# Performance work log

Measured on AMD Instinct MI355X. Metric: run time of the kernel, lower is better.

The kernel has to match this reference:

```python
import jax, jax.numpy as jnp
import numpy as np
from math import sqrt

B, T, C = 4, 2048, 2048
H = 16
D = C // H  # head_dim = 128


def setup_inputs() -> dict:
    key = jax.random.key(0)
    ks = jax.random.split(key, 7)
    s = 1.0 / sqrt(C)
    return {
        "querys": jax.random.normal(ks[0], (B, T, C), dtype=jnp.float32),
        "keys": jax.random.normal(ks[1], (B, T, C), dtype=jnp.float32),
        "values": jax.random.normal(ks[2], (B, T, C), dtype=jnp.float32),
        "Wq": jax.random.normal(ks[3], (C, C), dtype=jnp.float32) * s,
        "bq": jnp.zeros((C,), dtype=jnp.float32),
        "Wk": jax.random.normal(ks[4], (C, C), dtype=jnp.float32) * s,
        "bk": jnp.zeros((C,), dtype=jnp.float32),
        "Wv": jax.random.normal(ks[5], (C, C), dtype=jnp.float32) * s,
        "bv": jnp.zeros((C,), dtype=jnp.float32),
        "Wo": jax.random.normal(ks[6], (C, C), dtype=jnp.float32) * s,
        "bo": jnp.zeros((C,), dtype=jnp.float32),
        "is_causal": 1,
    }


def reference(querys, keys, values, Wq, bq, Wk, bk, Wv, bv, Wo, bo, is_causal):
    # Linear projections: x @ W^T + b (torch nn.Linear convention), here W stored as [C_in, C_out]
    q = (querys @ Wq + bq).reshape(B, T, H, D)
    k = (keys @ Wk + bk).reshape(B, T, H, D)
    v = (values @ Wv + bv).reshape(B, T, H, D)
    # scores: [B, H, T, T]
    scores = jnp.einsum("bqhd,bkhd->bhqk", q, k) / sqrt(D)
    if is_causal:
        mask = jnp.tril(jnp.ones((T, T), dtype=bool))  # allowed positions
        scores = jnp.where(mask, scores, -jnp.inf)
    weights = jax.nn.softmax(scores, axis=-1)
    attn = jnp.einsum("bhqk,bkhd->bqhd", weights, v).reshape(B, T, C)
    return attn @ Wo + bo
```

## Files before the change

### kernel.cpp

```cpp
#include <hip/hip_runtime.h>
#include <hip/hip_bf16.h>
#include <stdint.h>

#define BB 4
#define TT 2048
#define CC 2048
#define HH 16
#define DD 128
#define MM (BB*TT)

typedef __attribute__((ext_vector_type(8))) short bh8;
typedef __attribute__((ext_vector_type(4))) float fx4;

__device__ inline ushort f2bf(float x) {
    union { float f; uint32_t u; } c; c.f = x;
    uint32_t lsb = (c.u >> 16) & 1u;
    return (ushort)((c.u + 0x7fffu + lsb) >> 16);
}

__device__ inline void async16(const void* g, void* l) {
    __builtin_amdgcn_global_load_lds(
        (const __attribute__((address_space(1))) uint32_t*)g,
        (__attribute__((address_space(3))) uint32_t*)l, 16, 0, 0);
}

__global__ __launch_bounds__(256) void convert3_k(
    const float* __restrict__ i0, const float* __restrict__ i1,
    const float* __restrict__ i2,
    ushort* __restrict__ o0, ushort* __restrict__ o1, ushort* __restrict__ o2,
    int n)
{
    const float* in; ushort* out;
    switch (blockIdx.y) {
        case 0:  in = i0; out = o0; break;
        case 1:  in = i1; out = o1; break;
        default: in = i2; out = o2; break;
    }
    int i = (int)(blockIdx.x * 256 + threadIdx.x) * 4;
    if (i + 3 < n) {
        float4 v = *(const float4*)&in[i];
        ushort4 o;
        o.x = f2bf(v.x); o.y = f2bf(v.y); o.z = f2bf(v.z); o.w = f2bf(v.w);
        *(ushort4*)&out[i] = o;
    }
}

__global__ __launch_bounds__(256) void transpose4_w_k(
    const float* __restrict__ w0, const float* __restrict__ w1,
    const float* __restrict__ w2, const float* __restrict__ w3,
    ushort* __restrict__ t0, ushort* __restrict__ t1,
    ushort* __restrict__ t2, ushort* __restrict__ t3)
{
    const float* W; ushort* Wt;
    switch (blockIdx.z) {
        case 0:  W = w0; Wt = t0; break;
        case 1:  W = w1; Wt = t1; break;
        case 2:  W = w2; Wt = t2; break;
        default: W = w3; Wt = t3; break;
    }
    __shared__ __align__(16) ushort tile[32][33];
    const int n0 = blockIdx.x * 32, k0 = blockIdx.y * 32;
    const int tx = threadIdx.x, ty = threadIdx.y;
#pragma unroll
    for (int r = 0; r < 32; r += 8)
        tile[ty + r][tx] = f2bf(W[(size_t)(k0 + ty + r) * CC + n0 + tx]);
    __syncthreads();
    const int tid = ty * 32 + tx;
    const int p = tid & 15;
    const int row = tid >> 4;
#pragma unroll
    for (int rr = 0; rr < 2; ++rr) {
        const int n_row = row + rr * 16;
        ushort2 w2;
        w2.x = tile[2 * p][n_row];
        w2.y = tile[2 * p + 1][n_row];
        *(ushort2*)&Wt[(size_t)(n0 + n_row) * CC + k0 + 2 * p] = w2;
    }
}

template<int OUTF>
__device__ __forceinline__ void gemm_body(
    char (*Gsm)[65536],
    const ushort* A, const ushort* Bt, const float* bias, void* Cv, float osc)
{
    const int tid = (int)threadIdx.x;
    const int lane = tid & 63, wave = tid >> 6;
    const int fr = lane & 15, fg = lane >> 4;
    const int wm = wave >> 2, wn = wave & 3;

    const int bid = (int)blockIdx.x;
    const int xcd = bid & 7, local = bid >> 3;
    const int m_tile = xcd * 4 + (local >> 3);
    const int n_tile = local & 7;
    const int m0 = m_tile * 256, n0 = n_tile * 256;

    const ushort* Ag = A  + (size_t)m0 * CC;
    const ushort* Bg = Bt + (size_t)n0 * CC;
    const int nt = CC / 64;

    auto STAGE_G = [&](int t, int g) {
        if (t >= nt) return;
        const int khalf = g >> 1, isB = g & 1;
        char* base = Gsm[t & 1] + isB * 32768 + khalf * 16384;
        const ushort* src = isB ? Bg : Ag;
        const int kbase = t * 64 + khalf * 32;
#pragma unroll
        for (int l = 0; l < 2; ++l) {
            const int u = l * 512 + tid;
            const int j = u >> 3, s = u & 7;
            const int ek = s ^ (j & 7);
            const int e = (ek >> 2) & 1, ks = ek & 3;
            async16(src + (size_t)(2 * j + e) * CC + kbase + ks * 8,
                    base + u * 16);
        }
    };

    const int slot = ((((fr & 1) << 2) | fg) ^ ((fr >> 1) & 7));
    const int offA = (wm * 64 + (fr >> 1)) * 128 + slot * 16;
    const int offB = 32768 + (wn * 32 + (fr >> 1)) * 128 + slot * 16;

    fx4 acc[8][4];
#pragma unroll
    for (int i = 0; i < 8; ++i)
#pragma unroll
        for (int j = 0; j < 4; ++j)
            acc[i][j] = (fx4){0.f, 0.f, 0.f, 0.f};

#pragma unroll
    for (int g = 0; g < 4; ++g) STAGE_G(0, g);
    STAGE_G(1, 0);

#pragma unroll 1
    for (int t = 0; t < nt; ++t) {
        const char* kb = Gsm[t & 1];
#pragma unroll
        for (int kk = 0; kk < 2; ++kk) {
            if (kk == 0) {
                if (t == nt - 1) {
                    asm volatile("s_waitcnt vmcnt(0)" ::: "memory");
                } else {
                    asm volatile("s_waitcnt vmcnt(2)" ::: "memory");
                }
                __builtin_amdgcn_sched_barrier(0);
                __builtin_amdgcn_s_barrier();
                __builtin_amdgcn_sched_barrier(0);
            }

            const char* ka = kb + kk * 16384;
            const char* kbB = kb + kk * 16384;
            bh8 afr[4], bfr[4];

#pragma unroll
            for (int nf = 0; nf < 4; ++nf)
                bfr[nf] = *(const bh8*)(kbB + offB + nf * 1024);
#pragma unroll
            for (int i = 0; i < 4; ++i)
                afr[i] = *(const bh8*)(ka + offA + i * 1024);
            STAGE_G(t + 1, kk ? 3 : 1);

            __builtin_amdgcn_sched_barrier(0);
            __builtin_amdgcn_s_barrier();
            __builtin_amdgcn_sched_barrier(0);

            __builtin_amdgcn_s_setprio(1);
#pragma unroll
            for (int i = 0; i < 4; ++i)
#pragma unroll
                for (int nf = 0; nf < 4; ++nf)
                    acc[i][nf] = __builtin_amdgcn_mfma_f32_16x16x32_bf16(
                        afr[i], bfr[nf], acc[i][nf], 0, 0, 0);
            __builtin_amdgcn_s_setprio(0);

#pragma unroll
            for (int i = 0; i < 4; ++i)
                afr[i] = *(const bh8*)(ka + offA + (4 + i) * 1024);
            if (kk) STAGE_G(t + 2, 0);
            else    STAGE_G(t + 1, 2);

            __builtin_amdgcn_sched_barrier(0);
            __builtin_amdgcn_s_barrier();
            __builtin_amdgcn_sched_barrier(0);

            __builtin_amdgcn_s_setprio(1);
#pragma unroll
            for (int i = 0; i < 4; ++i)
#pragma unroll
                for (int nf = 0; nf < 4; ++nf)
                    acc[4 + i][nf] = __builtin_amdgcn_mfma_f32_16x16x32_bf16(
                        afr[i], bfr[nf], acc[4 + i][nf], 0, 0, 0);
            __builtin_amdgcn_s_setprio(0);
        }
    }

    if (OUTF == 2) {
        ushort* Vt = (ushort*)Cv;
#pragma unroll
        for (int nf = 0; nf < 4; ++nf) {
            const int col = n0 + wn * 64 + nf * 16 + fr;
            const int h = col >> 7, d = col & 127;
            const float bv = bias[col];
#pragma unroll
            for (int mfp = 0; mfp < 4; ++mfp) {
                const int rowb = m0 + wm * 128 + mfp * 32;
                const int b = rowb >> 11;
                const int tloc = (rowb & (TT - 1)) + fg * 8;
                union { ushort u[8]; uint4 v; } pk;
#pragma unroll
                for (int r = 0; r < 4; ++r) {
                    pk.u[r]     = f2bf(acc[2 * mfp][nf][r] + bv);
                    pk.u[4 + r] = f2bf(acc[2 * mfp + 1][nf][r] + bv);
                }
                *(uint4*)&Vt[((size_t)((b * HH + h) * DD + d)) * TT + tloc] = pk.v;
            }
        }
        return;
    }

#pragma unroll
    for (int nf = 0; nf < 4; ++nf) {
        const int col = n0 + wn * 64 + nf * 16 + fr;
        const float bv = bias[col];
#pragma unroll
        for (int mf = 0; mf < 8; ++mf) {
            const int row = m0 + wm * 128 + mf * 16 + fg * 4;
#pragma unroll
            for (int r = 0; r < 4; ++r) {
                float v = (acc[mf][nf][r] + bv) * osc;
                if (OUTF)
                    ((float*)Cv)[(size_t)(row + r) * CC + col] = v;
                else
                    ((ushort*)Cv)[(size_t)(row + r) * CC + col] = f2bf(v);
            }
        }
    }
}

__global__ __launch_bounds__(512, 2) void gemm_qkv_k(
    const ushort* __restrict__ Xq, const ushort* __restrict__ Xk,
    const ushort* __restrict__ Xv,
    const ushort* __restrict__ WqT, const ushort* __restrict__ WkT,
    const ushort* __restrict__ WvT,
    const float* __restrict__ bq, const float* __restrict__ bk,
    const float* __restrict__ bv,
    ushort* __restrict__ Qb, ushort* __restrict__ Kb, ushort* __restrict__ Vt)
{
    __shared__ __align__(16) char Gsm[2][65536];
    if (blockIdx.y == 0) {
        gemm_body<0>(Gsm, Xq, WqT, bq, Qb, 0.12751789836306614f);
    } else if (blockIdx.y == 1) {
        gemm_body<0>(Gsm, Xk, WkT, bk, Kb, 1.0f);
    } else {
        gemm_body<2>(Gsm, Xv, WvT, bv, Vt, 1.0f);
    }
}

__global__ __launch_bounds__(512, 2) void gemm_o_k(
    const ushort* __restrict__ A, const ushort* __restrict__ Bt,
    const float* __restrict__ bias, float* __restrict__ Cv)
{
    __shared__ __align__(16) char Gsm[2][65536];
    gemm_body<1>(Gsm, A, Bt, bias, Cv, 1.0f);
}

__global__ __launch_bounds__(512, 4) void flash_attn_k(
    const ushort* __restrict__ Qm, const ushort* __restrict__ Km,
    const ushort* __restrict__ Vt, ushort* __restrict__ Om,
    const int* __restrict__ causal_p)
{
    __shared__ __align__(16) char Ksm[2][16384];
    __shared__ __align__(16) char Vsm[2][16384];

    const int tid = (int)threadIdx.x;
    const int lane = tid & 63, wave = tid >> 6;
    const int fr = lane & 15, fg = lane >> 4;
    const int causal = causal_p[0];

    const int d_raw = (int)blockIdx.x + 8 * ((int)blockIdx.y + 16 * (int)blockIdx.z);
    const int xcd = d_raw & 7, jj = d_raw >> 3;
    const int head_lin = xcd * 8 + (jj & 7);
    const int pi = jj >> 3;
    const int h = head_lin & 15, b = head_lin >> 4;

    const ushort* Qp = Qm + (size_t)b * TT * CC + h * DD;
    const ushort* Kp = Km + (size_t)b * TT * CC + h * DD;
    const ushort* Vp = Vt + (size_t)(b * HH + h) * DD * TT;
    ushort* Op = Om + (size_t)b * TT * CC + h * DD;

    const bh8 onesf = {0x3F80, 0x3F80, 0x3F80, 0x3F80,
                       0x3F80, 0x3F80, 0x3F80, 0x3F80};

    auto STAGE = [&](int ti, int buf) {
        const int kv0 = ti * 64;
        {
            const int r0 = tid >> 4, s0 = tid & 15;
            async16(Kp + (size_t)(kv0 + r0) * CC + (s0 ^ (r0 & 15)) * 8,
                    Ksm[buf] + tid * 16);
            async16(Kp + (size_t)(kv0 + 32 + r0) * CC + (s0 ^ (r0 & 15)) * 8,
                    Ksm[buf] + 8192 + tid * 16);
        }
        {
            const int d0 = tid >> 3, s0 = tid & 7;
            async16(Vp + (size_t)d0 * TT + kv0 + (s0 ^ (d0 & 7)) * 8,
                    Vsm[buf] + tid * 16);
            async16(Vp + (size_t)(64 + d0) * TT + kv0 + (s0 ^ (d0 & 7)) * 8,
                    Vsm[buf] + 8192 + tid * 16);
        }
    };

#pragma unroll 1
    for (int pp = 0; pp < 2; ++pp) {
        const int tile = pp ? (15 - pi) : pi;
        const int q0 = tile * 128;
        const int qbase = q0 + wave * 16;
        const int q_idx = qbase + fr;

        bh8 qf[4];
#pragma unroll
        for (int s = 0; s < 4; ++s)
            qf[s] = *(const bh8*)&Qp[(size_t)(qbase + fr) * CC + s * 32 + fg * 8];

        fx4 o[8];
#pragma unroll
        for (int jn = 0; jn < 8; ++jn) o[jn] = (fx4){0.f, 0.f, 0.f, 0.f};
        fx4 o_l = (fx4){0.f, 0.f, 0.f, 0.f};

        const int nfull  = causal ? (q0 >> 6) : (TT / 64);
        const int ntiles = causal ? (nfull + 2) : (TT / 64);

        STAGE(0, 0);
#pragma unroll 1
        for (int t = 0; t < ntiles; ++t) {
            asm volatile("s_waitcnt vmcnt(0)" ::: "memory");
            __builtin_amdgcn_sched_barrier(0);
            __builtin_amdgcn_s_barrier();
            __builtin_amdgcn_sched_barrier(0);
            if (t + 1 < ntiles) STAGE(t + 1, (t + 1) & 1);

            const int kv0 = t * 64;
            const char* kb = Ksm[t & 1];
            const char* vb = Vsm[t & 1];
            const bool domask = causal && (t >= nfull);
            const bool active = !domask || (kv0 <= qbase + 15);

            if (active) {
                fx4 s4[4];
#pragma unroll
                for (int j = 0; j < 4; ++j) s4[j] = (fx4){0.f, 0.f, 0.f, 0.f};
                __builtin_amdgcn_s_setprio(1);
#pragma unroll
                for (int st = 0; st < 4; ++st) {
                    bh8 kf[4];
#pragma unroll
                    for (int j = 0; j < 4; ++j)
                        kf[j] = *(const bh8*)(kb + (j * 16 + fr) * 256 +
                                              ((st * 64 + fg * 16) ^ (fr << 4)));
#pragma unroll
                    for (int j = 0; j < 4; ++j)
                        s4[j] = __builtin_amdgcn_mfma_f32_16x16x32_bf16(
                            kf[j], qf[st], s4[j], 0, 0, 0);
                }
                __builtin_amdgcn_s_setprio(0);

#pragma unroll
                for (int g = 0; g < 2; ++g) {
                    float pg[2][4];
#pragma unroll
                    for (int j2 = 0; j2 < 2; ++j2) {
                        const int jb = g * 2 + j2;
#pragma unroll
                        for (int r = 0; r < 4; ++r) {
                            float v = s4[jb][r];
                            if (domask && (kv0 + jb * 16 + fg * 4 + r > q_idx))
                                v = -1e30f;
                            pg[j2][r] = exp2f(v);
                        }
                    }
                    union { uint u[4]; bh8 h; } pk;
                    asm("v_cvt_pk_bf16_f32 %0, %1, %2"
                        : "=v"(pk.u[0]) : "v"(pg[0][0]), "v"(pg[0][1]));
                    asm("v_cvt_pk_bf16_f32 %0, %1, %2"
                        : "=v"(pk.u[1]) : "v"(pg[0][2]), "v"(pg[0][3]));
                    asm("v_cvt_pk_bf16_f32 %0, %1, %2"
                        : "=v"(pk.u[2]) : "v"(pg[1][0]), "v"(pg[1][1]));
                    asm("v_cvt_pk_bf16_f32 %0, %1, %2"
                        : "=v"(pk.u[3]) : "v"(pg[1][2]), "v"(pg[1][3]));
                    const bh8 pf = pk.h;

                    o_l = __builtin_amdgcn_mfma_f32_16x16x32_bf16(
                        pf, onesf, o_l, 0, 0, 0);

                    __builtin_amdgcn_s_setprio(1);
#pragma unroll
                    for (int jn = 0; jn < 8; ++jn) {
                        bh8 vf = *(const bh8*)(vb + (jn * 16 + fr) * 128 +
                                               ((g * 64 + fg * 16) ^ ((fr & 7) << 4)));
                        o[jn] = __builtin_amdgcn_mfma_f32_16x16x32_bf16(
                            pf, vf, o[jn], 0, 0, 0);
                    }
                    __builtin_amdgcn_s_setprio(0);
                }
            }
        }

#pragma unroll
        for (int r = 0; r < 4; ++r) {
            const float inv = 1.0f / o_l[r];
            const size_t rowoff = (size_t)(qbase + fg * 4 + r) * CC;
#pragma unroll
            for (int jn = 0; jn < 8; ++jn)
                Op[rowoff + jn * 16 + fr] = f2bf(o[jn][r] * inv);
        }
    }
}

extern "C" void kernel_launch(void* const* d_in, const int* in_sizes, int n_in,
                              void* d_out, int out_size, void* d_ws, size_t ws_size,
                              hipStream_t stream)
{
    (void)in_sizes; (void)n_in; (void)out_size;
    const float* querys = (const float*)d_in[0];
    const float* keys   = (const float*)d_in[1];
    const float* values = (const float*)d_in[2];
    const float* Wq = (const float*)d_in[3];
    const float* bq = (const float*)d_in[4];
    const float* Wk = (const float*)d_in[5];
    const float* bk = (const float*)d_in[6];
    const float* Wv = (const float*)d_in[7];
    const float* bv = (const float*)d_in[8];
    const float* Wo = (const float*)d_in[9];
    const float* bo = (const float*)d_in[10];
    const int* is_causal = (const int*)d_in[11];

    const size_t WBYTES = (size_t)CC * CC * 2;
    const size_t XBYTES = (size_t)MM * CC * 2;
    if (ws_size < 4 * WBYTES + 4 * XBYTES) return;

    uint8_t* ws = (uint8_t*)d_ws;
    ushort* WqT = (ushort*)(ws);
    ushort* WkT = (ushort*)(ws + WBYTES);
    ushort* WvT = (ushort*)(ws + 2 * WBYTES);
    ushort* WoT = (ushort*)(ws + 3 * WBYTES);
    uint8_t* act = ws + 4 * WBYTES;
    ushort* Xq = (ushort*)(act);
    ushort* Xk = (ushort*)(act + XBYTES);
    ushort* Xv = (ushort*)(act + 2 * XBYTES);
    ushort* Qb = (ushort*)(act + 3 * XBYTES);
    ushort* Kb = Xq;
    ushort* Vt = Xk;
    ushort* Ob = Xv;

    dim3 tb(32, 8);
    transpose4_w_k<<<dim3(CC / 32, CC / 32, 4), tb, 0, stream>>>(
        Wq, Wk, Wv, Wo, WqT, WkT, WvT, WoT);

    const int nX = MM * CC;
    convert3_k<<<dim3(nX / 4 / 256, 3), 256, 0, stream>>>(
        querys, keys, values, Xq, Xk, Xv, nX);

    gemm_qkv_k<<<dim3((MM / 256) * (CC / 256), 3), 512, 0, stream>>>(
        Xq, Xk, Xv, WqT, WkT, WvT, bq, bk, bv, Qb, Kb, Vt);

    dim3 ga(8, HH, BB);
    flash_attn_k<<<ga, 512, 0, stream>>>(Qb, Kb, Vt, Ob, is_causal);

    gemm_o_k<<<dim3((MM / 256) * (CC / 256)), 512, 0, stream>>>(
        Ob, WoT, bo, (float*)d_out);
}
```

Before: 425.3 us.

## Process both paired causal tiles in a single KV sweep with 32 rows per wave

Instead of looping twice over the KV sequence (once for tile pi, once for tile 15-pi), waves 0-3 handle tile pi and waves 4-7 handle tile 15-pi in one shared sweep. Each wave now owns 32 query rows, so every K and V fragment read from LDS feeds two MFMAs. This removes the second round of KV staging for the short tile and improves LDS-to-MFMA reuse. In exchange, register use doubles for the accumulators, and the waves on the short tile sit idle through the later iterations of the sweep.

```diff
diff --git a/kernel.cpp b/kernel.cpp
--- a/kernel.cpp
+++ b/kernel.cpp
@@ -307,75 +307,89 @@
         }
     };
 
+    const int tile_sel = (wave < 4) ? pi : (15 - pi);
+    const int q0 = tile_sel * 128;
+    const int qbase = q0 + (wave & 3) * 32;
+
+    bh8 qf[2][4];
+#pragma unroll
+    for (int qq = 0; qq < 2; ++qq)
+#pragma unroll
+        for (int s = 0; s < 4; ++s)
+            qf[qq][s] = *(const bh8*)&Qp[(size_t)(qbase + qq * 16 + fr) * CC +
+                                         s * 32 + fg * 8];
+
+    fx4 o[2][8];
+#pragma unroll
+    for (int qq = 0; qq < 2; ++qq)
+#pragma unroll
+        for (int jn = 0; jn < 8; ++jn) o[qq][jn] = (fx4){0.f, 0.f, 0.f, 0.f};
+    fx4 o_l[2];
+    o_l[0] = (fx4){0.f, 0.f, 0.f, 0.f};
+    o_l[1] = (fx4){0.f, 0.f, 0.f, 0.f};
+
+    const int nt_sweep = causal ? ((15 - pi) * 2 + 2) : (TT / 64);
+    const int my_nfull = causal ? (q0 >> 6) : nt_sweep;
+    const int my_nt    = causal ? (my_nfull + 2) : nt_sweep;
+
+    STAGE(0, 0);
 #pragma unroll 1
-    for (int pp = 0; pp < 2; ++pp) {
-        const int tile = pp ? (15 - pi) : pi;
-        const int q0 = tile * 128;
-        const int qbase = q0 + wave * 16;
-        const int q_idx = qbase + fr;
-
-        bh8 qf[4];
-#pragma unroll
-        for (int s = 0; s < 4; ++s)
-            qf[s] = *(const bh8*)&Qp[(size_t)(qbase + fr) * CC + s * 32 + fg * 8];
-
-        fx4 o[8];
-#pragma unroll
-        for (int jn = 0; jn < 8; ++jn) o[jn] = (fx4){0.f, 0.f, 0.f, 0.f};
-        fx4 o_l = (fx4){0.f, 0.f, 0.f, 0.f};
-
-        const int nfull  = causal ? (q0 >> 6) : (TT / 64);
-        const int ntiles = causal ? (nfull + 2) : (TT / 64);
-
-        STAGE(0, 0);
-#pragma unroll 1
-        for (int t = 0; t < ntiles; ++t) {
-            asm volatile("s_waitcnt vmcnt(0)" ::: "memory");
-            __builtin_amdgcn_sched_barrier(0);
-            __builtin_amdgcn_s_barrier();
-            __builtin_amdgcn_sched_barrier(0);
-            if (t + 1 < ntiles) STAGE(t + 1, (t + 1) & 1);
-
-            const int kv0 = t * 64;
-            const char* kb = Ksm[t & 1];
-            const char* vb = Vsm[t & 1];
-            const bool domask = causal && (t >= nfull);
-            const bool active = !domask || (kv0 <= qbase + 15);
-
-            if (active) {
-                fx4 s4[4];
-#pragma unroll
-                for (int j = 0; j < 4; ++j) s4[j] = (fx4){0.f, 0.f, 0.f, 0.f};
-                __builtin_amdgcn_s_setprio(1);
-#pragma unroll
-                for (int st = 0; st < 4; ++st) {
-                    bh8 kf[4];
-#pragma unroll
-                    for (int j = 0; j < 4; ++j)
-                        kf[j] = *(const bh8*)(kb + (j * 16 + fr) * 256 +
-                                              ((st * 64 + fg * 16) ^ (fr << 4)));
-#pragma unroll
-                    for (int j = 0; j < 4; ++j)
-                        s4[j] = __builtin_amdgcn_mfma_f32_16x16x32_bf16(
-                            kf[j], qf[st], s4[j], 0, 0, 0);
+    for (int t = 0; t < nt_sweep; ++t) {
+        asm volatile("s_waitcnt vmcnt(0)" ::: "memory");
+        __builtin_amdgcn_sched_barrier(0);
+        __builtin_amdgcn_s_barrier();
+        __builtin_amdgcn_sched_barrier(0);
+        if (t + 1 < nt_sweep) STAGE(t + 1, (t + 1) & 1);
+
+        const int kv0 = t * 64;
+        const char* kb = Ksm[t & 1];
+        const char* vb = Vsm[t & 1];
+        const bool domask = causal && (t >= my_nfull);
+        const bool active = (t < my_nt) && (!domask || (kv0 <= qbase + 31));
+
+        if (active) {
+            fx4 s4[2][4];
+#pragma unroll
+            for (int qq = 0; qq < 2; ++qq)
+#pragma unroll
+                for (int j = 0; j < 4; ++j) s4[qq][j] = (fx4){0.f, 0.f, 0.f, 0.f};
+            __builtin_amdgcn_s_setprio(1);
+#pragma unroll
+            for (int st = 0; st < 4; ++st) {
+                bh8 kf[4];
+#pragma unroll
+                for (int j = 0; j < 4; ++j)
+                    kf[j] = *(const bh8*)(kb + (j * 16 + fr) * 256 +
+                                          ((st * 64 + fg * 16) ^ (fr << 4)));
+#pragma unroll
+                for (int j = 0; j < 4; ++j) {
+                    s4[0][j] = __builtin_amdgcn_mfma_f32_16x16x32_bf16(
+                        kf[j], qf[0][st], s4[0][j], 0, 0, 0);
+                    s4[1][j] = __builtin_amdgcn_mfma_f32_16x16x32_bf16(
+                        kf[j], qf[1][st], s4[1][j], 0, 0, 0);
                 }
-                __builtin_amdgcn_s_setprio(0);
-
-#pragma unroll
-                for (int g = 0; g < 2; ++g) {
+            }
+            __builtin_amdgcn_s_setprio(0);
+
+#pragma unroll
+            for (int g = 0; g < 2; ++g) {
+                bh8 pf[2];
+#pragma unroll
+                for (int qq = 0; qq < 2; ++qq) {
+                    const int q_idx = qbase + qq * 16 + fr;
                     float pg[2][4];
 #pragma unroll
                     for (int j2 = 0; j2 < 2; ++j2) {
                         const int jb = g * 2 + j2;
 #pragma unroll
                         for (int r = 0; r < 4; ++r) {
-                            float v = s4[jb][r];
+                            float v = s4[qq][jb][r];
                             if (domask && (kv0 + jb * 16 + fg * 4 + r > q_idx))
                                 v = -1e30f;
                             pg[j2][r] = exp2f(v);
                         }
                     }
-                    union { uint u[4]; bh8 h; } pk;
+                    union { uint u[4]; bh8 hh; } pk;
                     asm("v_cvt_pk_bf16_f32 %0, %1, %2"
                         : "=v"(pk.u[0]) : "v"(pg[0][0]), "v"(pg[0][1]));
                     asm("v_cvt_pk_bf16_f32 %0, %1, %2"
@@ -384,33 +398,36 @@
                         : "=v"(pk.u[2]) : "v"(pg[1][0]), "v"(pg[1][1]));
                     asm("v_cvt_pk_bf16_f32 %0, %1, %2"
                         : "=v"(pk.u[3]) : "v"(pg[1][2]), "v"(pg[1][3]));
-                    const bh8 pf = pk.h;
-
-                    o_l = __builtin_amdgcn_mfma_f32_16x16x32_bf16(
-                        pf, onesf, o_l, 0, 0, 0);
-
-                    __builtin_amdgcn_s_setprio(1);
-#pragma unroll
-                    for (int jn = 0; jn < 8; ++jn) {
-                        bh8 vf = *(const bh8*)(vb + (jn * 16 + fr) * 128 +
-                                               ((g * 64 + fg * 16) ^ ((fr & 7) << 4)));
-                        o[jn] = __builtin_amdgcn_mfma_f32_16x16x32_bf16(
-                            pf, vf, o[jn], 0, 0, 0);
-                    }
-                    __builtin_amdgcn_s_setprio(0);
+                    pf[qq] = pk.hh;
+                    o_l[qq] = __builtin_amdgcn_mfma_f32_16x16x32_bf16(
+                        pf[qq], onesf, o_l[qq], 0, 0, 0);
                 }
+
+                __builtin_amdgcn_s_setprio(1);
+#pragma unroll
+                for (int jn = 0; jn < 8; ++jn) {
+                    bh8 vf = *(const bh8*)(vb + (jn * 16 + fr) * 128 +
+                                           ((g * 64 + fg * 16) ^ ((fr & 7) << 4)));
+                    o[0][jn] = __builtin_amdgcn_mfma_f32_16x16x32_bf16(
+                        pf[0], vf, o[0][jn], 0, 0, 0);
+                    o[1][jn] = __builtin_amdgcn_mfma_f32_16x16x32_bf16(
+                        pf[1], vf, o[1][jn], 0, 0, 0);
+                }
+                __builtin_amdgcn_s_setprio(0);
             }
         }
-
+    }
+
+#pragma unroll
+    for (int qq = 0; qq < 2; ++qq)
 #pragma unroll
         for (int r = 0; r < 4; ++r) {
-            const float inv = 1.0f / o_l[r];
-            const size_t rowoff = (size_t)(qbase + fg * 4 + r) * CC;
+            const float inv = 1.0f / o_l[qq][r];
+            const size_t rowoff = (size_t)(qbase + qq * 16 + fg * 4 + r) * CC;
 #pragma unroll
             for (int jn = 0; jn < 8; ++jn)
-                Op[rowoff + jn * 16 + fr] = f2bf(o[jn][r] * inv);
-        }
-    }
+                Op[rowoff + jn * 16 + fr] = f2bf(o[qq][jn][r] * inv);
+        }
 }
 
 extern "C" void kernel_launch(void* const* d_in, const int* in_sizes, int n_in,
```

After: 583.3 us. +37.1%, slower.

## Fuse fp32-to-bf16 activation conversion into the QKV GEMM load path

Applied to the files above, without the earlier changes.

Removes the separate conversion kernel and has the QKV GEMM read fp32 activations directly into registers, convert them with packed bf16 instructions, and write the result into LDS, with the register loads software-pipelined across k-steps. This drops a full write and re-read of three bf16 activation copies. In exchange the GEMM reads twice as many A bytes (fp32) and uses register-staged loads instead of direct global-to-LDS loads, which adds register pressure and VALU/LDS-write work inside the main loop and changes the waitcnt accounting.

```diff
diff --git a/kernel.cpp b/kernel.cpp
--- a/kernel.cpp
+++ b/kernel.cpp
@@ -24,27 +24,6 @@
         (__attribute__((address_space(3))) uint32_t*)l, 16, 0, 0);
 }
 
-__global__ __launch_bounds__(256) void convert3_k(
-    const float* __restrict__ i0, const float* __restrict__ i1,
-    const float* __restrict__ i2,
-    ushort* __restrict__ o0, ushort* __restrict__ o1, ushort* __restrict__ o2,
-    int n)
-{
-    const float* in; ushort* out;
-    switch (blockIdx.y) {
-        case 0:  in = i0; out = o0; break;
-        case 1:  in = i1; out = o1; break;
-        default: in = i2; out = o2; break;
-    }
-    int i = (int)(blockIdx.x * 256 + threadIdx.x) * 4;
-    if (i + 3 < n) {
-        float4 v = *(const float4*)&in[i];
-        ushort4 o;
-        o.x = f2bf(v.x); o.y = f2bf(v.y); o.z = f2bf(v.z); o.w = f2bf(v.w);
-        *(ushort4*)&out[i] = o;
-    }
-}
-
 __global__ __launch_bounds__(256) void transpose4_w_k(
     const float* __restrict__ w0, const float* __restrict__ w1,
     const float* __restrict__ w2, const float* __restrict__ w3,
@@ -78,10 +57,10 @@
     }
 }
 
-template<int OUTF>
+template<int OUTF, int AF32>
 __device__ __forceinline__ void gemm_body(
     char (*Gsm)[65536],
-    const ushort* A, const ushort* Bt, const float* bias, void* Cv, float osc)
+    const void* Av, const ushort* Bt, const float* bias, void* Cv, float osc)
 {
     const int tid = (int)threadIdx.x;
     const int lane = tid & 63, wave = tid >> 6;
@@ -94,7 +73,8 @@
     const int n_tile = local & 7;
     const int m0 = m_tile * 256, n0 = n_tile * 256;
 
-    const ushort* Ag = A  + (size_t)m0 * CC;
+    const ushort* Ag16 = (const ushort*)Av + (size_t)m0 * CC;
+    const float*  Ag32 = (const float*)Av  + (size_t)m0 * CC;
     const ushort* Bg = Bt + (size_t)n0 * CC;
     const int nt = CC / 64;
 
@@ -102,7 +82,7 @@
         if (t >= nt) return;
         const int khalf = g >> 1, isB = g & 1;
         char* base = Gsm[t & 1] + isB * 32768 + khalf * 16384;
-        const ushort* src = isB ? Bg : Ag;
+        const ushort* src = isB ? Bg : Ag16;
         const int kbase = t * 64 + khalf * 32;
 #pragma unroll
         for (int l = 0; l < 2; ++l) {
@@ -115,6 +95,37 @@
         }
     };
 
+    const int aj = tid >> 3, as_ = tid & 7;
+    const int aek = as_ ^ (aj & 7);
+    const int ae = (aek >> 2) & 1, aks = aek & 3;
+    const int arow = 2 * aj + ae;
+    float4 pa0, pa1, pa2, pa3;
+
+    auto ISSUE_A = [&](int t, int khalf) {
+        if (!AF32 || t >= nt) return;
+        const float* s0 = Ag32 + (size_t)arow * CC + t * 64 + khalf * 32 + aks * 8;
+        pa0 = *(const float4*)s0;
+        pa1 = *(const float4*)(s0 + 4);
+        const float* s1 = s0 + (size_t)128 * CC;
+        pa2 = *(const float4*)s1;
+        pa3 = *(const float4*)(s1 + 4);
+    };
+    auto WRITE_A = [&](int t, int khalf) {
+        if (!AF32 || t >= nt) return;
+        char* base = Gsm[t & 1] + khalf * 16384;
+        union { uint q[4]; uint4 v; } w0, w1;
+        asm("v_cvt_pk_bf16_f32 %0, %1, %2" : "=v"(w0.q[0]) : "v"(pa0.x), "v"(pa0.y));
+        asm("v_cvt_pk_bf16_f32 %0, %1, %2" : "=v"(w0.q[1]) : "v"(pa0.z), "v"(pa0.w));
+        asm("v_cvt_pk_bf16_f32 %0, %1, %2" : "=v"(w0.q[2]) : "v"(pa1.x), "v"(pa1.y));
+        asm("v_cvt_pk_bf16_f32 %0, %1, %2" : "=v"(w0.q[3]) : "v"(pa1.z), "v"(pa1.w));
+        asm("v_cvt_pk_bf16_f32 %0, %1, %2" : "=v"(w1.q[0]) : "v"(pa2.x), "v"(pa2.y));
+        asm("v_cvt_pk_bf16_f32 %0, %1, %2" : "=v"(w1.q[1]) : "v"(pa2.z), "v"(pa2.w));
+        asm("v_cvt_pk_bf16_f32 %0, %1, %2" : "=v"(w1.q[2]) : "v"(pa3.x), "v"(pa3.y));
+        asm("v_cvt_pk_bf16_f32 %0, %1, %2" : "=v"(w1.q[3]) : "v"(pa3.z), "v"(pa3.w));
+        *(uint4*)(base + tid * 16) = w0.v;
+        *(uint4*)(base + 8192 + tid * 16) = w1.v;
+    };
+
     const int slot = ((((fr & 1) << 2) | fg) ^ ((fr >> 1) & 7));
     const int offA = (wm * 64 + (fr >> 1)) * 128 + slot * 16;
     const int offB = 32768 + (wn * 32 + (fr >> 1)) * 128 + slot * 16;
@@ -126,9 +137,16 @@
         for (int j = 0; j < 4; ++j)
             acc[i][j] = (fx4){0.f, 0.f, 0.f, 0.f};
 
-#pragma unroll
-    for (int g = 0; g < 4; ++g) STAGE_G(0, g);
-    STAGE_G(1, 0);
+    if (AF32) {
+        ISSUE_A(0, 0); WRITE_A(0, 0);
+        ISSUE_A(0, 1); WRITE_A(0, 1);
+        STAGE_G(0, 1); STAGE_G(0, 3);
+        ISSUE_A(1, 0);
+    } else {
+#pragma unroll
+        for (int g = 0; g < 4; ++g) STAGE_G(0, g);
+        STAGE_G(1, 0);
+    }
 
 #pragma unroll 1
     for (int t = 0; t < nt; ++t) {
@@ -136,10 +154,16 @@
 #pragma unroll
         for (int kk = 0; kk < 2; ++kk) {
             if (kk == 0) {
-                if (t == nt - 1) {
-                    asm volatile("s_waitcnt vmcnt(0)" ::: "memory");
+                if (AF32) {
+                    if (t == nt - 1)
+                        asm volatile("s_waitcnt vmcnt(0) lgkmcnt(0)" ::: "memory");
+                    else
+                        asm volatile("s_waitcnt vmcnt(4) lgkmcnt(0)" ::: "memory");
                 } else {
-                    asm volatile("s_waitcnt vmcnt(2)" ::: "memory");
+                    if (t == nt - 1)
+                        asm volatile("s_waitcnt vmcnt(0)" ::: "memory");
+                    else
+                        asm volatile("s_waitcnt vmcnt(2)" ::: "memory");
                 }
                 __builtin_amdgcn_sched_barrier(0);
                 __builtin_amdgcn_s_barrier();
@@ -156,6 +180,8 @@
 #pragma unroll
             for (int i = 0; i < 4; ++i)
                 afr[i] = *(const bh8*)(ka + offA + i * 1024);
+            if (kk == 0) WRITE_A(t + 1, 0);
+            else         WRITE_A(t + 1, 1);
             STAGE_G(t + 1, kk ? 3 : 1);
 
             __builtin_amdgcn_sched_barrier(0);
@@ -174,8 +200,12 @@
 #pragma unroll
             for (int i = 0; i < 4; ++i)
                 afr[i] = *(const bh8*)(ka + offA + (4 + i) * 1024);
-            if (kk) STAGE_G(t + 2, 0);
-            else    STAGE_G(t + 1, 2);
+            if (kk == 0) ISSUE_A(t + 1, 1);
+            else         ISSUE_A(t + 2, 0);
+            if (!AF32) {
+                if (kk) STAGE_G(t + 2, 0);
+                else    STAGE_G(t + 1, 2);
+            }
 
             __builtin_amdgcn_sched_barrier(0);
             __builtin_amdgcn_s_barrier();
@@ -236,8 +266,8 @@
 }
 
 __global__ __launch_bounds__(512, 2) void gemm_qkv_k(
-    const ushort* __restrict__ Xq, const ushort* __restrict__ Xk,
-    const ushort* __restrict__ Xv,
+    const float* __restrict__ Xq, const float* __restrict__ Xk,
+    const float* __restrict__ Xv,
     const ushort* __restrict__ WqT, const ushort* __restrict__ WkT,
     const ushort* __restrict__ WvT,
     const float* __restrict__ bq, const float* __restrict__ bk,
@@ -246,11 +276,11 @@
 {
     __shared__ __align__(16) char Gsm[2][65536];
     if (blockIdx.y == 0) {
-        gemm_body<0>(Gsm, Xq, WqT, bq, Qb, 0.12751789836306614f);
+        gemm_body<0, 1>(Gsm, Xq, WqT, bq, Qb, 0.12751789836306614f);
     } else if (blockIdx.y == 1) {
-        gemm_body<0>(Gsm, Xk, WkT, bk, Kb, 1.0f);
+        gemm_body<0, 1>(Gsm, Xk, WkT, bk, Kb, 1.0f);
     } else {
-        gemm_body<2>(Gsm, Xv, WvT, bv, Vt, 1.0f);
+        gemm_body<2, 1>(Gsm, Xv, WvT, bv, Vt, 1.0f);
     }
 }
 
@@ -259,7 +289,7 @@
     const float* __restrict__ bias, float* __restrict__ Cv)
 {
     __shared__ __align__(16) char Gsm[2][65536];
-    gemm_body<1>(Gsm, A, Bt, bias, Cv, 1.0f);
+    gemm_body<1, 0>(Gsm, A, Bt, bias, Cv, 1.0f);
 }
 
 __global__ __launch_bounds__(512, 4) void flash_attn_k(
@@ -441,24 +471,17 @@
     ushort* WvT = (ushort*)(ws + 2 * WBYTES);
     ushort* WoT = (ushort*)(ws + 3 * WBYTES);
     uint8_t* act = ws + 4 * WBYTES;
-    ushort* Xq = (ushort*)(act);
-    ushort* Xk = (ushort*)(act + XBYTES);
-    ushort* Xv = (ushort*)(act + 2 * XBYTES);
-    ushort* Qb = (ushort*)(act + 3 * XBYTES);
-    ushort* Kb = Xq;
-    ushort* Vt = Xk;
-    ushort* Ob = Xv;
+    ushort* Qb = (ushort*)(act);
+    ushort* Kb = (ushort*)(act + XBYTES);
+    ushort* Vt = (ushort*)(act + 2 * XBYTES);
+    ushort* Ob = (ushort*)(act + 3 * XBYTES);
 
     dim3 tb(32, 8);
     transpose4_w_k<<<dim3(CC / 32, CC / 32, 4), tb, 0, stream>>>(
         Wq, Wk, Wv, Wo, WqT, WkT, WvT, WoT);
 
-    const int nX = MM * CC;
-    convert3_k<<<dim3(nX / 4 / 256, 3), 256, 0, stream>>>(
-        querys, keys, values, Xq, Xk, Xv, nX);
-
     gemm_qkv_k<<<dim3((MM / 256) * (CC / 256), 3), 512, 0, stream>>>(
-        Xq, Xk, Xv, WqT, WkT, WvT, bq, bk, bv, Qb, Kb, Vt);
+        querys, keys, values, WqT, WkT, WvT, bq, bk, bv, Qb, Kb, Vt);
 
     dim3 ga(8, HH, BB);
     flash_attn_k<<<ga, 512, 0, stream>>>(Qb, Kb, Vt, Ob, is_causal);
```

Result: slower. 484.7 us (+14.0%).
